# Performance work log

Hardware: AMD Instinct MI355X
Metric: run time of the kernel (lower is better)

The kernel has to match this reference:

```python
import jax, jax.numpy as jnp
import numpy as np


def _conv3d(x, w, stride, pad):
    return jax.lax.conv_general_dilated(
        x, w, window_strides=stride, padding=[(p, p) for p in pad],
        dimension_numbers=('NCDHW', 'OIDHW', 'NCDHW'))


def _bn(x, g, b, eps=1e-5):
    # BatchNorm3d in training mode: batch statistics over (N, D, H, W)
    m = x.mean((0, 2, 3, 4), keepdims=True)
    v = ((x - m) ** 2).mean((0, 2, 3, 4), keepdims=True)
    return (x - m) * jax.lax.rsqrt(v + eps) * g.reshape(1, -1, 1, 1, 1) + b.reshape(1, -1, 1, 1, 1)


def _lrelu(x):
    return jnp.where(x >= 0, x, 0.2 * x)


def _deform_conv3d(x, off, w, stride, pad, n_off_groups):
    # Deformable conv3d: offsets predict per-output-location (dz,dy,dx) shifts for
    # every kernel tap, shared across channel groups of size C//n_off_groups.
    B, C, D, H, W = x.shape
    O, _, kd, kh, kw = w.shape
    K = kd * kh * kw
    sd, sh, sw = stride
    pd, ph, pw = pad
    Do = (D + 2 * pd - kd) // sd + 1
    Ho = (H + 2 * ph - kh) // sh + 1
    Wo = (W + 2 * pw - kw) // sw + 1
    G = n_off_groups
    Cg = C // G
    # offset layout: [B, G, K, 3(dz,dy,dx), Do, Ho, Wo]
    off = off.reshape(B, G, K, 3, Do, Ho, Wo)
    kz, ky, kx = jnp.meshgrid(jnp.arange(kd), jnp.arange(kh), jnp.arange(kw), indexing='ij')
    bz = (jnp.arange(Do) * sd - pd).astype(x.dtype)[:, None, None]
    by = (jnp.arange(Ho) * sh - ph).astype(x.dtype)[None, :, None]
    bx = (jnp.arange(Wo) * sw - pw).astype(x.dtype)[None, None, :]
    kb = lambda a: a.reshape(-1).astype(x.dtype)[None, None, :, None, None, None]
    pz = off[:, :, :, 0] + bz + kb(kz)   # [B,G,K,Do,Ho,Wo]
    py = off[:, :, :, 1] + by + kb(ky)
    px = off[:, :, :, 2] + bx + kb(kx)
    z0, y0, x0 = jnp.floor(pz), jnp.floor(py), jnp.floor(px)
    fz, fy, fx = pz - z0, py - y0, px - x0
    xg = x.reshape(B, G, Cg, D * H * W)
    acc = jnp.zeros((B, G, Cg, K, Do, Ho, Wo), x.dtype)
    for cz in (0, 1):
        for cy in (0, 1):
            for cx in (0, 1):
                zc, yc, xc = z0 + cz, y0 + cy, x0 + cx
                wgt = ((fz if cz else 1 - fz) * (fy if cy else 1 - fy) * (fx if cx else 1 - fx))
                valid = ((zc >= 0) & (zc <= D - 1) & (yc >= 0) & (yc <= H - 1)
                         & (xc >= 0) & (xc <= W - 1)).astype(x.dtype)
                zi = jnp.clip(zc, 0, D - 1).astype(jnp.int32)
                yi = jnp.clip(yc, 0, H - 1).astype(jnp.int32)
                xi = jnp.clip(xc, 0, W - 1).astype(jnp.int32)
                idx = ((zi * H + yi) * W + xi).reshape(B, G, 1, -1)
                v = jnp.take_along_axis(xg, jnp.broadcast_to(idx, (B, G, Cg, idx.shape[-1])), axis=3)
                acc = acc + (wgt * valid)[:, :, None] * v.reshape(B, G, Cg, K, Do, Ho, Wo)
    val = acc.reshape(B, C, K, Do, Ho, Wo)
    return jnp.einsum('bckdhw,ock->bodhw', val, w.reshape(O, C, K))


def setup_inputs() -> dict:
    key = jax.random.key(0)
    ks = jax.random.split(key, 24)
    f32 = jnp.float32
    p = lambda k, shape, s=0.05: jax.random.normal(k, shape, f32) * s
    gb = lambda k, c: (1.0 + 0.05 * jax.random.normal(k, (c,), f32),
                       0.05 * jax.random.normal(jax.random.fold_in(k, 1), (c,), f32))
    g2, b2 = gb(ks[8], 64)
    g3, b3 = gb(ks[9], 128)
    g4, b4 = gb(ks[10], 256)
    g5, b5 = gb(ks[11], 512)
    g6, b6 = gb(ks[12], 512)
    return {
        'input': jax.random.normal(ks[0], (64, 3, 8, 128, 128), f32),
        'w1': p(ks[1], (32, 3, 4, 4, 4)),
        'w2': p(ks[2], (64, 32, 2, 4, 4)),
        'w3': p(ks[3], (128, 64, 2, 4, 4)),
        'w4': p(ks[4], (256, 128, 1, 4, 4)),
        'w_off': p(ks[5], (192, 256, 1, 4, 4), 0.01),
        'w5': p(ks[6], (512, 256, 1, 4, 4)),
        'w6': p(ks[7], (512, 512, 1, 4, 4)),
        'g2': g2, 'b2': b2, 'g3': g3, 'b3': b3, 'g4': g4, 'b4': b4,
        'g5': g5, 'b5': b5, 'g6': g6, 'b6': b6,
    }


def reference(input, w1, w2, w3, w4, w_off, w5, w6,
              g2, b2, g3, b3, g4, b4, g5, b5, g6, b6):
    encs = []
    out = _lrelu(_conv3d(input, w1, (2, 2, 2), (1, 1, 1)))          # norm_1 unused in forward
    encs.append(out)
    out = _lrelu(_bn(_conv3d(out, w2, (1, 2, 2), (0, 1, 1)), g2, b2))
    encs.append(out)
    out = _lrelu(_bn(_conv3d(out, w3, (1, 2, 2), (0, 1, 1)), g3, b3))
    encs.append(out)
    out = _lrelu(_bn(_conv3d(out, w4, (1, 2, 2), (0, 1, 1)), g4, b4))
    encs.append(out)
    off = _conv3d(out, w_off, (1, 2, 2), (0, 1, 1))
    out = _lrelu(_bn(_deform_conv3d(out, off, w5, (1, 2, 2), (0, 1, 1), 4), g5, b5))
    encs.append(out)
    out = _lrelu(_bn(_conv3d(out, w6, (1, 1, 1), (0, 0, 0)), g6, b6))
    encs.append(out)
    return tuple(encs)
```

## Files before the change

kernel.cpp:

```cpp
#include <hip/hip_runtime.h>
#include <hip/hip_bf16.h>
#include <cstdint>

typedef short bf16x8 __attribute__((ext_vector_type(8)));
typedef float f32x4 __attribute__((ext_vector_type(4)));

__device__ __forceinline__ float lrelu_f(float y) { return y >= 0.f ? y : 0.2f * y; }
__device__ __forceinline__ float b2f(unsigned short u) {
    union { unsigned int i; float f; } v; v.i = ((unsigned int)u) << 16; return v.f;
}
__device__ __forceinline__ unsigned short f2b(float f) {
    union { unsigned int i; float f; } v; v.f = f;
    unsigned int r = v.i + 0x7FFFu + ((v.i >> 16) & 1u);
    return (unsigned short)(r >> 16);
}

__global__ __launch_bounds__(256) void xin_cl_k(const float* __restrict__ x,
                                                unsigned short* __restrict__ xc)
{
    int i = blockIdx.x * 256 + threadIdx.x;
    int c = i & 3, w = (i >> 2) & 127, h = (i >> 9) & 127, d = (i >> 16) & 7, b = i >> 19;
    float v = (c < 3) ? x[(((size_t)b * 3 + c) * 8 + d) * 16384 + h * 128 + w] : 0.f;
    xc[i] = f2b(v);
}

__global__ __launch_bounds__(256) void repack_w(const float* __restrict__ w,
                                                unsigned short* __restrict__ wp,
                                                int Cin, int Tap, int Cip, long total)
{
    long i = (long)blockIdx.x * 256 + threadIdx.x;
    if (i >= total) return;
    int c = (int)(i % Cip);
    long t1 = i / Cip;
    int t = (int)(t1 % Tap);
    long o = t1 / Tap;
    wp[i] = (c < Cin) ? f2b(w[((size_t)o * Cin + c) * Tap + t]) : (unsigned short)0;
}

__global__ __launch_bounds__(256) void f2bk(const float* __restrict__ in,
                                            unsigned short* __restrict__ o, long n)
{
    long i = (long)blockIdx.x * 256 + threadIdx.x;
    if (i < n) o[i] = f2b(in[i]);
}

template<int BN, int AMODE, int EPI>
__global__ __launch_bounds__(256) void igemm(
    const unsigned short* __restrict__ A, const unsigned short* __restrict__ Bw,
    void* __restrict__ Cout,
    int M, int N, int K, int klen,
    int Ci, int Di, int Hi, int Wi,
    int kd, int kh, int kw,
    int sd, int sh_, int sw_, int pd, int ph_, int pw_,
    int Do, int Ho, int Wo)
{
    constexpr int NF = BN / 32;
    constexpr int WN = 16 * NF;
    constexpr int NBU = (BN * 4 + 255) / 256;
    __shared__ __align__(16) unsigned short As[4][128][8];
    __shared__ __align__(16) unsigned short Bs[4][BN][8];
    const int tid = threadIdx.x;
    const int m0 = blockIdx.x * 128;
    const int n0 = blockIdx.y * BN;
    const int k0 = blockIdx.z * klen;
    const int kend = min(K, k0 + klen);

    size_t bsrc[NBU];
    unsigned short* bdst[NBU];
#pragma unroll
    for (int i = 0; i < NBU; ++i) {
        int u = tid + i * 256;
        int row = u >> 2, s = u & 3;
        if (BN * 4 >= 256 || u < BN * 4) {
            bsrc[i] = (size_t)(n0 + row) * K + s * 8;
            bdst[i] = &Bs[s][row][0];
        }
    }

    constexpr int NAU = (AMODE == 2) ? 4 : 2;
    size_t asz[2];
    int asrc[NAU];
    unsigned long long amask[NAU];
    unsigned short* adst[NAU];

    if constexpr (AMODE == 0) {
#pragma unroll
        for (int i = 0; i < 2; ++i) {
            int u = tid + i * 256;
            int r = u >> 2, s = u & 3;
            asz[i] = (size_t)(m0 + r) * K + s * 8;
            adst[i] = &As[s][r][0];
        }
    } else {
#pragma unroll
        for (int i = 0; i < NAU; ++i) {
            int u = tid + i * 256;
            int r = (AMODE == 2) ? (u >> 3) : (u >> 2);
            int m = m0 + r;
            int ow = m % Wo; int t1 = m / Wo;
            int oh = t1 % Ho; t1 /= Ho;
            int od = t1 % Do; int b = t1 / Do;
            int id0 = od * sd - pd, ih0 = oh * sh_ - ph_, iw0 = ow * sw_ - pw_;
            unsigned long long xm = 0ull, yx = 0ull, mask = 0ull;
            for (int p = 0; p < kw; ++p) if ((unsigned)(iw0 + p) < (unsigned)Wi) xm |= 1ull << p;
            for (int p = 0; p < kh; ++p) if ((unsigned)(ih0 + p) < (unsigned)Hi) yx |= xm << (p * kw);
            for (int p = 0; p < kd; ++p) if ((unsigned)(id0 + p) < (unsigned)Di) mask |= yx << (p * kh * kw);
            amask[i] = mask;
            int bsp = ((b * Di + id0) * Hi + ih0) * Wi + iw0;
            if constexpr (AMODE == 1) {
                int s = u & 3;
                asrc[i] = bsp * Ci + s * 8;
                adst[i] = &As[s][r][0];
            } else {
                int j = u & 7;
                asrc[i] = (bsp + (j >> 2) * Wi + (j & 3)) * 4;
                adst[i] = &As[j >> 1][r][(j & 1) * 4];
            }
        }
    }

    f32x4 acc[4][NF];
#pragma unroll
    for (int i = 0; i < 4; ++i)
#pragma unroll
        for (int j = 0; j < NF; ++j) acc[i][j] = (f32x4){0.f, 0.f, 0.f, 0.f};

    const int lane = tid & 63, wv = tid >> 6;
    const int wm = wv >> 1, wn = wv & 1;
    const int kg = lane >> 4, fr = lane & 15;

    int c0 = 0, kx = 0, ky = 0, tap = 0, doff = 0;
    if constexpr (AMODE == 1) {
        c0 = k0 % Ci;
        tap = k0 / Ci;
        kx = tap % kw;
        int t2 = tap / kw;
        ky = t2 % kh;
        int kz = t2 / kh;
        doff = (kz * Hi + ky) * Wi + kx;
    }

    for (int k = k0; k < kend; k += 32) {
#pragma unroll
        for (int i = 0; i < NBU; ++i)
            if (BN * 4 >= 256 || tid + i * 256 < BN * 4) {
                uint4 v = *(const uint4*)&Bw[bsrc[i] + k];
                *(uint4*)bdst[i] = v;
            }
        if constexpr (AMODE == 0) {
#pragma unroll
            for (int i = 0; i < 2; ++i) {
                uint4 v = *(const uint4*)&A[asz[i] + k];
                *(uint4*)adst[i] = v;
            }
        } else if constexpr (AMODE == 1) {
            int dofe = doff * Ci + c0;
#pragma unroll
            for (int i = 0; i < 2; ++i) {
                uint4 v = {0u, 0u, 0u, 0u};
                if ((amask[i] >> tap) & 1ull)
                    v = *(const uint4*)&A[(size_t)(asrc[i] + dofe)];
                *(uint4*)adst[i] = v;
            }
        } else {
            int kz = k >> 6;
            int U4 = (kz * (Hi * Wi) + ((k >> 5) & 1) * 2 * Wi) * 4;
            int tap0 = k >> 2;
#pragma unroll
            for (int i = 0; i < 4; ++i) {
                int j = (tid + i * 256) & 7;
                uint2 v = {0u, 0u};
                if ((amask[i] >> (tap0 + j)) & 1ull)
                    v = *(const uint2*)&A[(size_t)(asrc[i] + U4)];
                *(uint2*)adst[i] = v;
            }
        }
        __syncthreads();
        bf16x8 af[4], bfr[NF];
#pragma unroll
        for (int mi = 0; mi < 4; ++mi)
            af[mi] = *(const bf16x8*)&As[kg][wm * 64 + mi * 16 + fr][0];
#pragma unroll
        for (int ni = 0; ni < NF; ++ni)
            bfr[ni] = *(const bf16x8*)&Bs[kg][wn * WN + ni * 16 + fr][0];
#pragma unroll
        for (int mi = 0; mi < 4; ++mi)
#pragma unroll
            for (int ni = 0; ni < NF; ++ni)
                acc[mi][ni] = __builtin_amdgcn_mfma_f32_16x16x32_bf16(af[mi], bfr[ni], acc[mi][ni], 0, 0, 0);
        __syncthreads();
        if constexpr (AMODE == 1) {
            c0 += 32;
            if (c0 >= Ci) {
                c0 = 0; ++tap; ++kx; ++doff;
                if (kx == kw) {
                    kx = 0; doff += Wi - kw; ++ky;
                    if (ky == kh) { ky = 0; doff += (Hi - kh) * Wi; }
                }
            }
        }
    }
    const int rb = m0 + wm * 64 + (lane >> 4) * 4;
    const int cb = n0 + wn * WN + fr;
#pragma unroll
    for (int mi = 0; mi < 4; ++mi)
#pragma unroll
        for (int ni = 0; ni < NF; ++ni)
#pragma unroll
            for (int rg = 0; rg < 4; ++rg) {
                size_t idx = (size_t)(rb + mi * 16 + rg) * N + cb + ni * 16;
                float vv = acc[mi][ni][rg];
                if constexpr (EPI == 0) ((unsigned short*)Cout)[idx] = f2b(vv);
                else if constexpr (EPI == 1) ((float*)Cout)[idx] = vv;
                else if constexpr (EPI == 2) atomicAdd((float*)Cout + idx, vv);
                else ((unsigned short*)Cout)[idx] = f2b(lrelu_f(vv));
            }
}

__global__ __launch_bounds__(256) void bn_sums(const unsigned short* __restrict__ x,
                                               float* __restrict__ sums,
                                               long totalSlots, int C)
{
    const int tid = threadIdx.x;
    long gid = (long)blockIdx.x * 256 + tid;
    long stride = (long)gridDim.x * 256;
    float s1[8], s2[8];
#pragma unroll
    for (int j = 0; j < 8; ++j) { s1[j] = 0.f; s2[j] = 0.f; }
    for (long s = gid; s < totalSlots; s += stride) {
        uint4 v = *(const uint4*)&x[s * 8];
        const unsigned short* pv = (const unsigned short*)&v;
#pragma unroll
        for (int j = 0; j < 8; ++j) { float f = b2f(pv[j]); s1[j] += f; s2[j] += f * f; }
    }
    __shared__ float r1[2048], r2[2048];
#pragma unroll
    for (int j = 0; j < 8; ++j) { r1[tid * 8 + j] = s1[j]; r2[tid * 8 + j] = s2[j]; }
    __syncthreads();
    int G = C >> 3;
    for (int c = tid; c < C; c += 256) {
        int grp = c >> 3, j = c & 7;
        float a = 0.f, b = 0.f;
        for (int th = grp; th < 256; th += G) { a += r1[th * 8 + j]; b += r2[th * 8 + j]; }
        atomicAdd(&sums[c], a);
        atomicAdd(&sums[C + c], b);
    }
}

__global__ __launch_bounds__(256) void bn_fin(const float* __restrict__ sums,
                                              const float* __restrict__ g, const float* __restrict__ bt,
                                              float* __restrict__ sc, float* __restrict__ sh,
                                              int C, float invcnt)
{
    int c = blockIdx.x * 256 + threadIdx.x;
    if (c >= C) return;
    float mean = sums[c] * invcnt;
    float var = sums[C + c] * invcnt - mean * mean;
    float rs = rsqrtf(var + 1e-5f);
    float scl = g[c] * rs;
    sc[c] = scl;
    sh[c] = bt[c] - mean * scl;
}

template<int MODE>
__global__ __launch_bounds__(256) void bn_apply_t(
    unsigned short* __restrict__ x, const float* __restrict__ sc, const float* __restrict__ sh,
    float* __restrict__ outN, int C, int TC, int S)
{
    __shared__ __align__(16) float T[64][68];
    const int tid = threadIdx.x;
    const long m0 = (long)blockIdx.x * 64;
    const int c0 = blockIdx.y * TC;
    const int spr = TC >> 3;
    const int lg = (spr == 8) ? 3 : 2;
    const int tot = 64 * spr;
    for (int u = tid; u < tot; u += 256) {
        int r = u >> lg, sl = u & (spr - 1);
        size_t idx = (size_t)(m0 + r) * C + c0 + sl * 8;
        uint4 v = *(uint4*)&x[idx];
        unsigned short* pv = (unsigned short*)&v;
#pragma unroll
        for (int j = 0; j < 8; ++j) {
            int c = c0 + sl * 8 + j;
            float f = b2f(pv[j]);
            if (MODE == 1) {
                f = lrelu_f(f * sc[c] + sh[c]);
                pv[j] = f2b(f);
            }
            T[sl * 8 + j][r] = f;
        }
        if (MODE == 1) *(uint4*)&x[idx] = v;
    }
    __syncthreads();
    const int tpc = 256 / TC;
    const int rpt = 64 / tpc;
    int cl = tid / tpc;
    int r0 = (tid % tpc) * rpt;
    int c = c0 + cl;
    if ((S & 63) == 0) {
        long b = m0 / S;
        long s0 = m0 - b * S;
        float* op = outN + ((size_t)b * C + c) * S + s0 + r0;
        for (int r = 0; r < rpt; r += 4)
            *(float4*)(op + r) = *(float4*)&T[cl][r0 + r];
    } else {
        for (int r = 0; r < rpt; ++r) {
            long m = m0 + r0 + r;
            long b = m / S, s = m - b * S;
            outN[((size_t)b * C + c) * S + s] = T[cl][r0 + r];
        }
    }
}

__global__ __launch_bounds__(256) void deform_val(
    const unsigned short* __restrict__ xcl, const float* __restrict__ offc,
    unsigned short* __restrict__ val)
{
    int bs = blockIdx.x;
    int b = bs >> 5, s = bs & 31;
    int od = s >> 4, oh = (s >> 2) & 3, ow = s & 3;
    __shared__ float cw[64][8];
    __shared__ int cidx[64][8];
    int tid = threadIdx.x;
    if (tid < 64) {
        int gk = tid, k = gk & 15;
        int ky = k >> 2, kx = k & 3;
        const float* op = offc + (size_t)bs * 192 + gk * 3;
        float pz = op[0] + (float)od;
        float py = op[1] + (float)(oh * 2 - 1 + ky);
        float px = op[2] + (float)(ow * 2 - 1 + kx);
        float z0 = floorf(pz), y0 = floorf(py), x0 = floorf(px);
        float fz = pz - z0, fy = py - y0, fx = px - x0;
#pragma unroll
        for (int ci = 0; ci < 8; ++ci) {
            int cz = ci >> 2, cy = (ci >> 1) & 1, cx = ci & 1;
            float zc = z0 + cz, yc = y0 + cy, xc = x0 + cx;
            bool ok = zc >= 0.f && zc <= 1.f && yc >= 0.f && yc <= 7.f && xc >= 0.f && xc <= 7.f;
            int zi = min(max((int)zc, 0), 1);
            int yi = min(max((int)yc, 0), 7);
            int xi = min(max((int)xc, 0), 7);
            float wz = cz ? fz : 1.f - fz;
            float wy = cy ? fy : 1.f - fy;
            float wx = cx ? fx : 1.f - fx;
            cw[gk][ci] = ok ? wz * wy * wx : 0.f;
            cidx[gk][ci] = (zi * 8 + yi) * 8 + xi;
        }
    }
    __syncthreads();
    const unsigned short* xb = xcl + (size_t)b * 128 * 256;
    unsigned short* vo = val + (size_t)bs * 4096;
    for (int j = tid; j < 4096; j += 256) {
        int c = j & 255, tap = j >> 8;
        int gk = ((c >> 6) << 4) | tap;
        float v = 0.f;
#pragma unroll
        for (int i = 0; i < 8; ++i)
            v += cw[gk][i] * b2f(xb[(size_t)cidx[gk][i] * 256 + c]);
        vo[j] = f2b(v);
    }
}

extern "C" void kernel_launch(void* const* d_in, const int* in_sizes, int n_in,
                              void* d_out, int out_size, void* d_ws, size_t ws_size,
                              hipStream_t stream)
{
    (void)in_sizes; (void)n_in; (void)out_size; (void)ws_size;
    const float* x     = (const float*)d_in[0];
    const float* w1    = (const float*)d_in[1];
    const float* w2    = (const float*)d_in[2];
    const float* w3    = (const float*)d_in[3];
    const float* w4    = (const float*)d_in[4];
    const float* w_off = (const float*)d_in[5];
    const float* w5    = (const float*)d_in[6];
    const float* w6    = (const float*)d_in[7];
    const float* g2 = (const float*)d_in[8];  const float* b2 = (const float*)d_in[9];
    const float* g3 = (const float*)d_in[10]; const float* b3 = (const float*)d_in[11];
    const float* g4 = (const float*)d_in[12]; const float* b4 = (const float*)d_in[13];
    const float* g5 = (const float*)d_in[14]; const float* b5 = (const float*)d_in[15];
    const float* g6 = (const float*)d_in[16]; const float* b6 = (const float*)d_in[17];

    float* out = (float*)d_out;
    float* enc0 = out;
    float* enc1 = out + 33554432;
    float* enc2 = out + 46137344;
    float* enc3 = out + 50331648;
    float* enc4 = out + 52428800;
    float* enc5 = out + 53477376;

    char* W = (char*)d_ws;
    unsigned short* w1p  = (unsigned short*)(W + 0);
    unsigned short* w2p  = (unsigned short*)(W + 16384);
    unsigned short* w3p  = (unsigned short*)(W + 147456);
    unsigned short* w4p  = (unsigned short*)(W + 671744);
    unsigned short* wofp = (unsigned short*)(W + 1720320);
    unsigned short* w5p  = (unsigned short*)(W + 3293184);
    unsigned short* w6p  = (unsigned short*)(W + 7487488);
    float* sums          = (float*)(W + 15876096);
    float* sc            = (float*)(W + 15880192);
    float* sh            = (float*)(W + 15882240);
    float* offc          = (float*)(W + 15884288);
    unsigned short* xcl  = (unsigned short*)(W + 17457152);
    unsigned short* e1c  = (unsigned short*)(W + 17457152);
    unsigned short* e2c  = (unsigned short*)(W + 42622976);
    unsigned short* e3c  = (unsigned short*)(W + 51011584);
    unsigned short* e0c  = (unsigned short*)(W + 84566016);
    unsigned short* valb = (unsigned short*)(W + 84566016);
    float* raw5          = (float*)(W + 101343232);
    unsigned short* e4c  = (unsigned short*)(W + 105537536);
    float* raw6          = (float*)(W + 107634688);
    unsigned short* e5c  = (unsigned short*)(W + 107896832);

    xin_cl_k<<<131072, 256, 0, stream>>>(x, xcl);
    repack_w<<<32, 256, 0, stream>>>(w1, w1p, 3, 64, 4, 8192L);
    repack_w<<<256, 256, 0, stream>>>(w2, w2p, 32, 32, 32, 65536L);
    repack_w<<<1024, 256, 0, stream>>>(w3, w3p, 64, 32, 64, 262144L);
    repack_w<<<2048, 256, 0, stream>>>(w4, w4p, 128, 16, 128, 524288L);
    repack_w<<<3072, 256, 0, stream>>>(w_off, wofp, 256, 16, 256, 786432L);
    repack_w<<<8192, 256, 0, stream>>>(w5, w5p, 256, 16, 256, 2097152L);
    repack_w<<<16384, 256, 0, stream>>>(w6, w6p, 512, 16, 512, 4194304L);

    igemm<32, 2, 3><<<dim3(8192, 1, 1), 256, 0, stream>>>(
        xcl, w1p, e0c, 1048576, 32, 256, 256,
        4, 8, 128, 128, 4, 4, 4, 2, 2, 2, 1, 1, 1, 4, 64, 64);
    bn_apply_t<0><<<dim3(16384, 1), 256, 0, stream>>>(e0c, nullptr, nullptr, enc0, 32, 32, 16384);

    igemm<64, 1, 0><<<dim3(1536, 1, 1), 256, 0, stream>>>(
        e0c, w2p, e1c, 196608, 64, 1024, 1024,
        32, 4, 64, 64, 2, 4, 4, 1, 2, 2, 0, 1, 1, 3, 32, 32);
    hipMemsetAsync(sums, 0, 4096, stream);
    bn_sums<<<256, 256, 0, stream>>>(e1c, sums, 1572864L, 64);
    bn_fin<<<1, 256, 0, stream>>>(sums, g2, b2, sc, sh, 64, 1.f / 196608.f);
    bn_apply_t<1><<<dim3(3072, 1), 256, 0, stream>>>(e1c, sc, sh, enc1, 64, 64, 3072);

    igemm<128, 1, 0><<<dim3(256, 1, 1), 256, 0, stream>>>(
        e1c, w3p, e2c, 32768, 128, 2048, 2048,
        64, 3, 32, 32, 2, 4, 4, 1, 2, 2, 0, 1, 1, 2, 16, 16);
    hipMemsetAsync(sums, 0, 4096, stream);
    bn_sums<<<256, 256, 0, stream>>>(e2c, sums, 524288L, 128);
    bn_fin<<<1, 256, 0, stream>>>(sums, g3, b3, sc, sh, 128, 1.f / 32768.f);
    bn_apply_t<1><<<dim3(512, 2), 256, 0, stream>>>(e2c, sc, sh, enc2, 128, 64, 512);

    igemm<64, 1, 0><<<dim3(64, 4), 256, 0, stream>>>(
        e2c, w4p, e3c, 8192, 256, 2048, 2048,
        128, 2, 16, 16, 1, 4, 4, 1, 2, 2, 0, 1, 1, 2, 8, 8);
    hipMemsetAsync(sums, 0, 4096, stream);
    bn_sums<<<256, 256, 0, stream>>>(e3c, sums, 262144L, 256);
    bn_fin<<<1, 256, 0, stream>>>(sums, g4, b4, sc, sh, 256, 1.f / 8192.f);
    bn_apply_t<1><<<dim3(128, 4), 256, 0, stream>>>(e3c, sc, sh, enc3, 256, 64, 128);

    hipMemsetAsync(offc, 0, 1572864, stream);
    igemm<64, 1, 2><<<dim3(16, 3, 8), 256, 0, stream>>>(
        e3c, wofp, offc, 2048, 192, 4096, 512,
        256, 2, 8, 8, 1, 4, 4, 1, 2, 2, 0, 1, 1, 2, 4, 4);

    deform_val<<<2048, 256, 0, stream>>>(e3c, offc, valb);
    hipMemsetAsync(raw5, 0, 4194304, stream);
    igemm<64, 0, 2><<<dim3(16, 8, 4), 256, 0, stream>>>(
        valb, w5p, raw5, 2048, 512, 4096, 1024,
        0, 0, 0, 0, 1, 1, 1, 1, 1, 1, 0, 0, 0, 1, 1, 1);
    f2bk<<<4096, 256, 0, stream>>>(raw5, e4c, 1048576L);
    hipMemsetAsync(sums, 0, 4096, stream);
    bn_sums<<<256, 256, 0, stream>>>(e4c, sums, 131072L, 512);
    bn_fin<<<2, 256, 0, stream>>>(sums, g5, b5, sc, sh, 512, 1.f / 2048.f);
    bn_apply_t<1><<<dim3(32, 8), 256, 0, stream>>>(e4c, sc, sh, enc4, 512, 64, 32);

    hipMemsetAsync(raw6, 0, 262144, stream);
    igemm<64, 0, 2><<<dim3(1, 8, 16), 256, 0, stream>>>(
        e4c, w6p, raw6, 128, 512, 8192, 512,
        0, 0, 0, 0, 1, 1, 1, 1, 1, 1, 0, 0, 0, 1, 1, 1);
    f2bk<<<256, 256, 0, stream>>>(raw6, e5c, 65536L);
    hipMemsetAsync(sums, 0, 4096, stream);
    bn_sums<<<256, 256, 0, stream>>>(e5c, sums, 8192L, 512);
    bn_fin<<<2, 256, 0, stream>>>(sums, g6, b6, sc, sh, 512, 1.f / 128.f);
    bn_apply_t<1><<<dim3(2, 8), 256, 0, stream>>>(e5c, sc, sh, enc5, 512, 64, 2);
}
```

Baseline: 650.2 us.

## Store activations in spatially zero-padded layout to drop bounds masks in conv loads

Intermediate channels-last activations are now stored with a one-pixel zero border in H and W (and D for the input), written by the GEMM epilogue and bn_apply via padded row indexing, with new zero_border kernels clearing the halos. The implicit-GEMM A-loads for the strided convs (new AMODE 3 and a reworked AMODE 2) then skip per-tap validity masks and read unconditionally with wider uint4 loads for the first layer. This removes branchy, masked gather logic and the mask setup, at the cost of larger buffers, extra border-zeroing launches, per-row index arithmetic in the epilogues, and bn_sums reading the padded zeros. That last point relies on the borders being zero so the channel sums stay correct while the original counts are kept.

```diff
diff --git a/kernel.cpp b/kernel.cpp
--- a/kernel.cpp
+++ b/kernel.cpp
@@ -19,8 +19,18 @@
                                                 unsigned short* __restrict__ xc)
 {
     int i = blockIdx.x * 256 + threadIdx.x;
-    int c = i & 3, w = (i >> 2) & 127, h = (i >> 9) & 127, d = (i >> 16) & 7, b = i >> 19;
-    float v = (c < 3) ? x[(((size_t)b * 3 + c) * 8 + d) * 16384 + h * 128 + w] : 0.f;
+    int c = i & 3;
+    int sp = i >> 2;
+    int w = sp % 130;
+    int t = sp / 130;
+    int h = t % 130;
+    int t2 = t / 130;
+    int d = t2 % 10;
+    int b = t2 / 10;
+    int wr = w - 1, hr = h - 1, dr = d - 1;
+    float v = 0.f;
+    if (c < 3 && (unsigned)wr < 128u && (unsigned)hr < 128u && (unsigned)dr < 8u)
+        v = x[(((size_t)b * 3 + c) * 8 + dr) * 16384 + hr * 128 + wr];
     xc[i] = f2b(v);
 }
 
@@ -44,7 +54,25 @@
     if (i < n) o[i] = f2b(in[i]);
 }
 
-template<int BN, int AMODE, int EPI>
+__global__ __launch_bounds__(256) void zero_border(unsigned short* __restrict__ buf,
+                                                   int planes, int Hp, int Wp, int C)
+{
+    int perim = 2 * Wp + 2 * (Hp - 2);
+    int total = planes * perim;
+    int i = blockIdx.x * 256 + threadIdx.x;
+    if (i >= total) return;
+    int p = i % perim;
+    int pl = i / perim;
+    int h, w;
+    if (p < Wp) { h = 0; w = p; }
+    else if (p < 2 * Wp) { h = Hp - 1; w = p - Wp; }
+    else { int q = p - 2 * Wp; h = 1 + (q >> 1); w = (q & 1) ? (Wp - 1) : 0; }
+    unsigned short* dst = buf + ((size_t)(pl * Hp + h) * Wp + w) * C;
+    uint4 z = {0u, 0u, 0u, 0u};
+    for (int c = 0; c < C; c += 8) *(uint4*)(dst + c) = z;
+}
+
+template<int BN, int AMODE, int EPI, int OP>
 __global__ __launch_bounds__(256) void igemm(
     const unsigned short* __restrict__ A, const unsigned short* __restrict__ Bw,
     void* __restrict__ Cout,
@@ -77,11 +105,10 @@
         }
     }
 
-    constexpr int NAU = (AMODE == 2) ? 4 : 2;
     size_t asz[2];
-    int asrc[NAU];
-    unsigned long long amask[NAU];
-    unsigned short* adst[NAU];
+    int asrc[2];
+    unsigned long long amask[2];
+    unsigned short* adst[2];
 
     if constexpr (AMODE == 0) {
 #pragma unroll
@@ -91,31 +118,40 @@
             asz[i] = (size_t)(m0 + r) * K + s * 8;
             adst[i] = &As[s][r][0];
         }
+    } else if constexpr (AMODE == 2) {
+#pragma unroll
+        for (int i = 0; i < 2; ++i) {
+            int u = tid + i * 256;
+            int r = u >> 2, s = u & 3;
+            int m = m0 + r;
+            int ow = m % Wo; int t1 = m / Wo;
+            int oh = t1 % Ho; t1 /= Ho;
+            int od = t1 % Do; int b = t1 / Do;
+            int id0 = od * sd, ih0 = oh * sh_, iw0 = ow * sw_;
+            int bsp = ((b * Di + id0) * Hi + ih0) * Wi + iw0;
+            asrc[i] = (bsp + (s >> 1) * Wi + (s & 1) * 2) * 4;
+            adst[i] = &As[s][r][0];
+        }
     } else {
 #pragma unroll
-        for (int i = 0; i < NAU; ++i) {
+        for (int i = 0; i < 2; ++i) {
             int u = tid + i * 256;
-            int r = (AMODE == 2) ? (u >> 3) : (u >> 2);
+            int r = u >> 2, s = u & 3;
             int m = m0 + r;
             int ow = m % Wo; int t1 = m / Wo;
             int oh = t1 % Ho; t1 /= Ho;
             int od = t1 % Do; int b = t1 / Do;
             int id0 = od * sd - pd, ih0 = oh * sh_ - ph_, iw0 = ow * sw_ - pw_;
-            unsigned long long xm = 0ull, yx = 0ull, mask = 0ull;
-            for (int p = 0; p < kw; ++p) if ((unsigned)(iw0 + p) < (unsigned)Wi) xm |= 1ull << p;
-            for (int p = 0; p < kh; ++p) if ((unsigned)(ih0 + p) < (unsigned)Hi) yx |= xm << (p * kw);
-            for (int p = 0; p < kd; ++p) if ((unsigned)(id0 + p) < (unsigned)Di) mask |= yx << (p * kh * kw);
-            amask[i] = mask;
+            if constexpr (AMODE == 1) {
+                unsigned long long xm = 0ull, yx = 0ull, mask = 0ull;
+                for (int p = 0; p < kw; ++p) if ((unsigned)(iw0 + p) < (unsigned)Wi) xm |= 1ull << p;
+                for (int p = 0; p < kh; ++p) if ((unsigned)(ih0 + p) < (unsigned)Hi) yx |= xm << (p * kw);
+                for (int p = 0; p < kd; ++p) if ((unsigned)(id0 + p) < (unsigned)Di) mask |= yx << (p * kh * kw);
+                amask[i] = mask;
+            }
             int bsp = ((b * Di + id0) * Hi + ih0) * Wi + iw0;
-            if constexpr (AMODE == 1) {
-                int s = u & 3;
-                asrc[i] = bsp * Ci + s * 8;
-                adst[i] = &As[s][r][0];
-            } else {
-                int j = u & 7;
-                asrc[i] = (bsp + (j >> 2) * Wi + (j & 3)) * 4;
-                adst[i] = &As[j >> 1][r][(j & 1) * 4];
-            }
+            asrc[i] = bsp * Ci + s * 8;
+            adst[i] = &As[s][r][0];
         }
     }
 
@@ -130,7 +166,7 @@
     const int kg = lane >> 4, fr = lane & 15;
 
     int c0 = 0, kx = 0, ky = 0, tap = 0, doff = 0;
-    if constexpr (AMODE == 1) {
+    if constexpr (AMODE == 1 || AMODE == 3) {
         c0 = k0 % Ci;
         tap = k0 / Ci;
         kx = tap % kw;
@@ -153,6 +189,15 @@
                 uint4 v = *(const uint4*)&A[asz[i] + k];
                 *(uint4*)adst[i] = v;
             }
+        } else if constexpr (AMODE == 2) {
+            int kz = k >> 6;
+            int ky0 = (k >> 4) & 3;
+            int U = (kz * (Hi * Wi) + ky0 * Wi) * 4;
+#pragma unroll
+            for (int i = 0; i < 2; ++i) {
+                uint4 v = *(const uint4*)&A[(size_t)(asrc[i] + U)];
+                *(uint4*)adst[i] = v;
+            }
         } else if constexpr (AMODE == 1) {
             int dofe = doff * Ci + c0;
 #pragma unroll
@@ -163,16 +208,11 @@
                 *(uint4*)adst[i] = v;
             }
         } else {
-            int kz = k >> 6;
-            int U4 = (kz * (Hi * Wi) + ((k >> 5) & 1) * 2 * Wi) * 4;
-            int tap0 = k >> 2;
-#pragma unroll
-            for (int i = 0; i < 4; ++i) {
-                int j = (tid + i * 256) & 7;
-                uint2 v = {0u, 0u};
-                if ((amask[i] >> (tap0 + j)) & 1ull)
-                    v = *(const uint2*)&A[(size_t)(asrc[i] + U4)];
-                *(uint2*)adst[i] = v;
+            int dofe = doff * Ci + c0;
+#pragma unroll
+            for (int i = 0; i < 2; ++i) {
+                uint4 v = *(const uint4*)&A[(size_t)(asrc[i] + dofe)];
+                *(uint4*)adst[i] = v;
             }
         }
         __syncthreads();
@@ -189,7 +229,7 @@
             for (int ni = 0; ni < NF; ++ni)
                 acc[mi][ni] = __builtin_amdgcn_mfma_f32_16x16x32_bf16(af[mi], bfr[ni], acc[mi][ni], 0, 0, 0);
         __syncthreads();
-        if constexpr (AMODE == 1) {
+        if constexpr (AMODE == 1 || AMODE == 3) {
             c0 += 32;
             if (c0 >= Ci) {
                 c0 = 0; ++tap; ++kx; ++doff;
@@ -205,16 +245,28 @@
 #pragma unroll
     for (int mi = 0; mi < 4; ++mi)
 #pragma unroll
-        for (int ni = 0; ni < NF; ++ni)
-#pragma unroll
-            for (int rg = 0; rg < 4; ++rg) {
-                size_t idx = (size_t)(rb + mi * 16 + rg) * N + cb + ni * 16;
+        for (int rg = 0; rg < 4; ++rg) {
+            int mr = rb + mi * 16 + rg;
+            size_t rowbase;
+            if constexpr (OP == 1) {
+                int ow = mr % Wo; int t1 = mr / Wo;
+                int oh = t1 % Ho; t1 /= Ho;
+                int od = t1 % Do; int b = t1 / Do;
+                size_t prow = ((size_t)(b * Do + od) * (Ho + 2) + oh + 1) * (Wo + 2) + ow + 1;
+                rowbase = prow * N;
+            } else {
+                rowbase = (size_t)mr * N;
+            }
+#pragma unroll
+            for (int ni = 0; ni < NF; ++ni) {
+                size_t idx = rowbase + cb + ni * 16;
                 float vv = acc[mi][ni][rg];
                 if constexpr (EPI == 0) ((unsigned short*)Cout)[idx] = f2b(vv);
                 else if constexpr (EPI == 1) ((float*)Cout)[idx] = vv;
                 else if constexpr (EPI == 2) atomicAdd((float*)Cout + idx, vv);
                 else ((unsigned short*)Cout)[idx] = f2b(lrelu_f(vv));
             }
+        }
 }
 
 __global__ __launch_bounds__(256) void bn_sums(const unsigned short* __restrict__ x,
@@ -265,18 +317,29 @@
 template<int MODE>
 __global__ __launch_bounds__(256) void bn_apply_t(
     unsigned short* __restrict__ x, const float* __restrict__ sc, const float* __restrict__ sh,
-    float* __restrict__ outN, int C, int TC, int S)
+    float* __restrict__ outN, int C, int TC, int Do, int Ho, int Wo, int PAD)
 {
     __shared__ __align__(16) float T[64][68];
     const int tid = threadIdx.x;
-    const long m0 = (long)blockIdx.x * 64;
+    const int m0 = blockIdx.x * 64;
     const int c0 = blockIdx.y * TC;
+    const int S = Do * Ho * Wo;
     const int spr = TC >> 3;
     const int lg = (spr == 8) ? 3 : 2;
     const int tot = 64 * spr;
     for (int u = tid; u < tot; u += 256) {
         int r = u >> lg, sl = u & (spr - 1);
-        size_t idx = (size_t)(m0 + r) * C + c0 + sl * 8;
+        int m = m0 + r;
+        size_t prow;
+        if (PAD) {
+            int ow = m % Wo; int t1 = m / Wo;
+            int oh = t1 % Ho; t1 /= Ho;
+            int od = t1 % Do; int b = t1 / Do;
+            prow = ((size_t)(b * Do + od) * (Ho + 2) + oh + 1) * (Wo + 2) + ow + 1;
+        } else {
+            prow = m;
+        }
+        size_t idx = prow * C + c0 + sl * 8;
         uint4 v = *(uint4*)&x[idx];
         unsigned short* pv = (unsigned short*)&v;
 #pragma unroll
@@ -298,8 +361,8 @@
     int r0 = (tid % tpc) * rpt;
     int c = c0 + cl;
     if ((S & 63) == 0) {
-        long b = m0 / S;
-        long s0 = m0 - b * S;
+        long b = (long)m0 / S;
+        long s0 = (long)m0 - b * S;
         float* op = outN + ((size_t)b * C + c) * S + s0 + r0;
         for (int r = 0; r < rpt; r += 4)
             *(float4*)(op + r) = *(float4*)&T[cl][r0 + r];
@@ -343,11 +406,11 @@
             float wy = cy ? fy : 1.f - fy;
             float wx = cx ? fx : 1.f - fx;
             cw[gk][ci] = ok ? wz * wy * wx : 0.f;
-            cidx[gk][ci] = (zi * 8 + yi) * 8 + xi;
+            cidx[gk][ci] = zi * 100 + yi * 10 + xi + 11;
         }
     }
     __syncthreads();
-    const unsigned short* xb = xcl + (size_t)b * 128 * 256;
+    const unsigned short* xb = xcl + (size_t)b * 51200;
     unsigned short* vo = val + (size_t)bs * 4096;
     for (int j = tid; j < 4096; j += 256) {
         int c = j & 255, tap = j >> 8;
@@ -399,18 +462,22 @@
     float* sc            = (float*)(W + 15880192);
     float* sh            = (float*)(W + 15882240);
     float* offc          = (float*)(W + 15884288);
-    unsigned short* xcl  = (unsigned short*)(W + 17457152);
     unsigned short* e1c  = (unsigned short*)(W + 17457152);
-    unsigned short* e2c  = (unsigned short*)(W + 42622976);
-    unsigned short* e3c  = (unsigned short*)(W + 51011584);
-    unsigned short* e0c  = (unsigned short*)(W + 84566016);
-    unsigned short* valb = (unsigned short*)(W + 84566016);
-    float* raw5          = (float*)(W + 101343232);
-    unsigned short* e4c  = (unsigned short*)(W + 105537536);
-    float* raw6          = (float*)(W + 107634688);
-    unsigned short* e5c  = (unsigned short*)(W + 107896832);
-
-    xin_cl_k<<<131072, 256, 0, stream>>>(x, xcl);
+    unsigned short* e2c  = (unsigned short*)(W + 45867008);
+    unsigned short* e3c  = (unsigned short*)(W + 56483840);
+    unsigned short* e4c  = (unsigned short*)(W + 63037440);
+    float* raw6          = (float*)(W + 65134592);
+    unsigned short* e5c  = (unsigned short*)(W + 65396736);
+    unsigned short* valb = (unsigned short*)(W + 65527808);
+    float* raw5          = (float*)(W + 82305024);
+    unsigned short* xcl  = (unsigned short*)(W + 86499328);
+    unsigned short* e0c  = (unsigned short*)(W + 173027328);
+
+    zero_border<<<260, 256, 0, stream>>>(e0c, 256, 66, 66, 32);
+    zero_border<<<99, 256, 0, stream>>>(e1c, 192, 34, 34, 64);
+    zero_border<<<34, 256, 0, stream>>>(e2c, 128, 18, 18, 128);
+    zero_border<<<18, 256, 0, stream>>>(e3c, 128, 10, 10, 256);
+    xin_cl_k<<<169000, 256, 0, stream>>>(x, xcl);
     repack_w<<<32, 256, 0, stream>>>(w1, w1p, 3, 64, 4, 8192L);
     repack_w<<<256, 256, 0, stream>>>(w2, w2p, 32, 32, 32, 65536L);
     repack_w<<<1024, 256, 0, stream>>>(w3, w3p, 64, 32, 64, 262144L);
@@ -419,58 +486,58 @@
     repack_w<<<8192, 256, 0, stream>>>(w5, w5p, 256, 16, 256, 2097152L);
     repack_w<<<16384, 256, 0, stream>>>(w6, w6p, 512, 16, 512, 4194304L);
 
-    igemm<32, 2, 3><<<dim3(8192, 1, 1), 256, 0, stream>>>(
+    igemm<32, 2, 3, 1><<<dim3(8192, 1, 1), 256, 0, stream>>>(
         xcl, w1p, e0c, 1048576, 32, 256, 256,
-        4, 8, 128, 128, 4, 4, 4, 2, 2, 2, 1, 1, 1, 4, 64, 64);
-    bn_apply_t<0><<<dim3(16384, 1), 256, 0, stream>>>(e0c, nullptr, nullptr, enc0, 32, 32, 16384);
-
-    igemm<64, 1, 0><<<dim3(1536, 1, 1), 256, 0, stream>>>(
+        4, 10, 130, 130, 4, 4, 4, 2, 2, 2, 0, 0, 0, 4, 64, 64);
+    bn_apply_t<0><<<dim3(16384, 1), 256, 0, stream>>>(e0c, nullptr, nullptr, enc0, 32, 32, 4, 64, 64, 1);
+
+    igemm<64, 3, 0, 1><<<dim3(1536, 1, 1), 256, 0, stream>>>(
         e0c, w2p, e1c, 196608, 64, 1024, 1024,
-        32, 4, 64, 64, 2, 4, 4, 1, 2, 2, 0, 1, 1, 3, 32, 32);
+        32, 4, 66, 66, 2, 4, 4, 1, 2, 2, 0, 0, 0, 3, 32, 32);
     hipMemsetAsync(sums, 0, 4096, stream);
-    bn_sums<<<256, 256, 0, stream>>>(e1c, sums, 1572864L, 64);
+    bn_sums<<<256, 256, 0, stream>>>(e1c, sums, 1775616L, 64);
     bn_fin<<<1, 256, 0, stream>>>(sums, g2, b2, sc, sh, 64, 1.f / 196608.f);
-    bn_apply_t<1><<<dim3(3072, 1), 256, 0, stream>>>(e1c, sc, sh, enc1, 64, 64, 3072);
-
-    igemm<128, 1, 0><<<dim3(256, 1, 1), 256, 0, stream>>>(
+    bn_apply_t<1><<<dim3(3072, 1), 256, 0, stream>>>(e1c, sc, sh, enc1, 64, 64, 3, 32, 32, 1);
+
+    igemm<128, 3, 0, 1><<<dim3(256, 1, 1), 256, 0, stream>>>(
         e1c, w3p, e2c, 32768, 128, 2048, 2048,
-        64, 3, 32, 32, 2, 4, 4, 1, 2, 2, 0, 1, 1, 2, 16, 16);
+        64, 3, 34, 34, 2, 4, 4, 1, 2, 2, 0, 0, 0, 2, 16, 16);
     hipMemsetAsync(sums, 0, 4096, stream);
-    bn_sums<<<256, 256, 0, stream>>>(e2c, sums, 524288L, 128);
+    bn_sums<<<256, 256, 0, stream>>>(e2c, sums, 663552L, 128);
     bn_fin<<<1, 256, 0, stream>>>(sums, g3, b3, sc, sh, 128, 1.f / 32768.f);
-    bn_apply_t<1><<<dim3(512, 2), 256, 0, stream>>>(e2c, sc, sh, enc2, 128, 64, 512);
-
-    igemm<64, 1, 0><<<dim3(64, 4), 256, 0, stream>>>(
+    bn_apply_t<1><<<dim3(512, 2), 256, 0, stream>>>(e2c, sc, sh, enc2, 128, 64, 2, 16, 16, 1);
+
+    igemm<64, 3, 0, 1><<<dim3(64, 4), 256, 0, stream>>>(
         e2c, w4p, e3c, 8192, 256, 2048, 2048,
-        128, 2, 16, 16, 1, 4, 4, 1, 2, 2, 0, 1, 1, 2, 8, 8);
+        128, 2, 18, 18, 1, 4, 4, 1, 2, 2, 0, 0, 0, 2, 8, 8);
     hipMemsetAsync(sums, 0, 4096, stream);
-    bn_sums<<<256, 256, 0, stream>>>(e3c, sums, 262144L, 256);
+    bn_sums<<<256, 256, 0, stream>>>(e3c, sums, 409600L, 256);
     bn_fin<<<1, 256, 0, stream>>>(sums, g4, b4, sc, sh, 256, 1.f / 8192.f);
-    bn_apply_t<1><<<dim3(128, 4), 256, 0, stream>>>(e3c, sc, sh, enc3, 256, 64, 128);
+    bn_apply_t<1><<<dim3(128, 4), 256, 0, stream>>>(e3c, sc, sh, enc3, 256, 64, 2, 8, 8, 1);
 
     hipMemsetAsync(offc, 0, 1572864, stream);
-    igemm<64, 1, 2><<<dim3(16, 3, 8), 256, 0, stream>>>(
+    igemm<64, 3, 2, 0><<<dim3(16, 3, 8), 256, 0, stream>>>(
         e3c, wofp, offc, 2048, 192, 4096, 512,
-        256, 2, 8, 8, 1, 4, 4, 1, 2, 2, 0, 1, 1, 2, 4, 4);
+        256, 2, 10, 10, 1, 4, 4, 1, 2, 2, 0, 0, 0, 2, 4, 4);
 
     deform_val<<<2048, 256, 0, stream>>>(e3c, offc, valb);
     hipMemsetAsync(raw5, 0, 4194304, stream);
-    igemm<64, 0, 2><<<dim3(16, 8, 4), 256, 0, stream>>>(
+    igemm<64, 0, 2, 0><<<dim3(16, 8, 4), 256, 0, stream>>>(
         valb, w5p, raw5, 2048, 512, 4096, 1024,
         0, 0, 0, 0, 1, 1, 1, 1, 1, 1, 0, 0, 0, 1, 1, 1);
     f2bk<<<4096, 256, 0, stream>>>(raw5, e4c, 1048576L);
     hipMemsetAsync(sums, 0, 4096, stream);
     bn_sums<<<256, 256, 0, stream>>>(e4c, sums, 131072L, 512);
     bn_fin<<<2, 256, 0, stream>>>(sums, g5, b5, sc, sh, 512, 1.f / 2048.f);
-    bn_apply_t<1><<<dim3(32, 8), 256, 0, stream>>>(e4c, sc, sh, enc4, 512, 64, 32);
+    bn_apply_t<1><<<dim3(32, 8), 256, 0, stream>>>(e4c, sc, sh, enc4, 512, 64, 2, 4, 4, 0);
 
     hipMemsetAsync(raw6, 0, 262144, stream);
-    igemm<64, 0, 2><<<dim3(1, 8, 16), 256, 0, stream>>>(
+    igemm<64, 0, 2, 0><<<dim3(1, 8, 16), 256, 0, stream>>>(
         e4c, w6p, raw6, 128, 512, 8192, 512,
         0, 0, 0, 0, 1, 1, 1, 1, 1, 1, 0, 0, 0, 1, 1, 1);
     f2bk<<<256, 256, 0, stream>>>(raw6, e5c, 65536L);
     hipMemsetAsync(sums, 0, 4096, stream);
     bn_sums<<<256, 256, 0, stream>>>(e5c, sums, 8192L, 512);
     bn_fin<<<2, 256, 0, stream>>>(sums, g6, b6, sc, sh, 512, 1.f / 128.f);
-    bn_apply_t<1><<<dim3(2, 8), 256, 0, stream>>>(e5c, sc, sh, enc5, 512, 64, 2);
-}
+    bn_apply_t<1><<<dim3(2, 8), 256, 0, stream>>>(e5c, sc, sh, enc5, 512, 64, 2, 1, 1, 0);
+}
```

New measurement: 711.6 us. 1.09x slower.
